# Optimization experiments

Hardware: AMD Instinct MI355X
Metric: run time of the kernel (lower is better)

## Reference

```python
import jax, jax.numpy as jnp
import numpy as np

BEAM_WIDTH = 5  # degenerate: all beams share the same per-step topk, so best beam == greedy argmax path
BLANK = 0


def setup_inputs() -> dict:
    key = jax.random.key(0)
    N, C, T = 128, 128, 2048
    logits = jax.random.normal(key, (N, C, T), dtype=jnp.float32)
    return {"logits": logits}


def reference(logits) -> jnp.ndarray:
    # (N, C, T) -> (N, T, C), log-softmax over classes (matches F.log_softmax(dim=2))
    log_probs = jax.nn.log_softmax(jnp.transpose(logits, (0, 2, 1)), axis=2)
    N, T, C = log_probs.shape
    # Beam search in the source is degenerate: every beam expands with the identical
    # per-timestep top-k, so the highest-scoring beam is exactly the per-step argmax.
    tokens = jnp.argmax(log_probs, axis=2).astype(jnp.int32)  # (N, T)
    # CTC-style collapse (decode()): drop blanks and repeated tokens.
    prev = jnp.concatenate([jnp.full((N, 1), -1, dtype=jnp.int32), tokens[:, :-1]], axis=1)
    keep = (tokens != BLANK) & (tokens != prev)  # (N, T) bool
    # Left-compact kept tokens into a blank-padded (N, T) output.
    pos = jnp.cumsum(keep, axis=1) - 1            # target position if kept
    pos = jnp.where(keep, pos, T)                 # dropped tokens -> dump slot T
    out = jnp.full((N, T + 1), BLANK, dtype=jnp.int32)
    out = out.at[jnp.arange(N)[:, None], pos].set(tokens)
    return out[:, :T]
```

## Files before the change

kernel.cpp:

```cpp
#include <hip/hip_runtime.h>


constexpr int N = 128;
constexpr int C = 128;
constexpr int T = 2048;

__global__ __launch_bounds__(256) void argmax_kernel(const float* __restrict__ logits,
                                                     int* __restrict__ tokens) {
    __shared__ float sb[3][4][64];
    __shared__ int   si[3][4][64];

    const int tid = threadIdx.x;
    const int tq  = tid & 63;
    const int grp = tid >> 6;
    const int b   = blockIdx.x;
    const int n   = b >> 3;
    const int t4  = (b & 7) * 256 + tq * 4;

    const float* base = logits + (size_t)n * C * T + (size_t)(grp * 32) * T + t4;

    float4 best = make_float4(-__builtin_inff(), -__builtin_inff(),
                              -__builtin_inff(), -__builtin_inff());
    int4 bidx = make_int4(0, 0, 0, 0);

    #pragma unroll
    for (int cc = 0; cc < 32; cc += 8) {
        float4 v[8];
        #pragma unroll
        for (int j = 0; j < 8; ++j)
            v[j] = *(const float4*)(base + (size_t)(cc + j) * T);
        #pragma unroll
        for (int j = 0; j < 8; ++j) {
            const int c = cc + j;
            if (v[j].x > best.x) { best.x = v[j].x; bidx.x = c; }
            if (v[j].y > best.y) { best.y = v[j].y; bidx.y = c; }
            if (v[j].z > best.z) { best.z = v[j].z; bidx.z = c; }
            if (v[j].w > best.w) { best.w = v[j].w; bidx.w = c; }
        }
    }

    if (grp > 0) {
        sb[grp - 1][0][tq] = best.x; si[grp - 1][0][tq] = bidx.x + grp * 32;
        sb[grp - 1][1][tq] = best.y; si[grp - 1][1][tq] = bidx.y + grp * 32;
        sb[grp - 1][2][tq] = best.z; si[grp - 1][2][tq] = bidx.z + grp * 32;
        sb[grp - 1][3][tq] = best.w; si[grp - 1][3][tq] = bidx.w + grp * 32;
    }
    __syncthreads();
    if (grp == 0) {
        #pragma unroll
        for (int g = 0; g < 3; ++g) {
            float f;
            f = sb[g][0][tq]; if (f > best.x) { best.x = f; bidx.x = si[g][0][tq]; }
            f = sb[g][1][tq]; if (f > best.y) { best.y = f; bidx.y = si[g][1][tq]; }
            f = sb[g][2][tq]; if (f > best.z) { best.z = f; bidx.z = si[g][2][tq]; }
            f = sb[g][3][tq]; if (f > best.w) { best.w = f; bidx.w = si[g][3][tq]; }
        }
        *(int4*)(tokens + (size_t)n * T + t4) = bidx;
    }
}

__global__ __launch_bounds__(256) void collapse_kernel(const int* __restrict__ tokens,
                                                       int* __restrict__ out) {
    const int n = blockIdx.x;
    const int* trow = tokens + (size_t)n * T;
    int* orow = out + (size_t)n * T;
    const int tid = threadIdx.x;
    constexpr int PER = T / 256;
    const int t0 = tid * PER;

    int tok[PER];
    *(int4*)&tok[0] = *(const int4*)(trow + t0);
    *(int4*)&tok[4] = *(const int4*)(trow + t0 + 4);
    int prev = (t0 == 0) ? -1 : trow[t0 - 1];

    int kpos[PER];
    int cnt = 0;
    #pragma unroll
    for (int i = 0; i < PER; ++i) {
        const bool k = (tok[i] != 0) && (tok[i] != prev);
        kpos[i] = k ? cnt : -1;
        cnt += k ? 1 : 0;
        prev = tok[i];
    }

    const int lane = tid & 63;
    const int wid  = tid >> 6;
    int incl = cnt;
    #pragma unroll
    for (int d = 1; d < 64; d <<= 1) {
        int v = __shfl_up(incl, d, 64);
        if (lane >= d) incl += v;
    }

    __shared__ int wsum[4];
    if (lane == 63) wsum[wid] = incl;

    const int4 z = make_int4(0, 0, 0, 0);
    *(int4*)(orow + t0)     = z;
    *(int4*)(orow + t0 + 4) = z;

    __syncthreads();

    int wbase = 0;
    #pragma unroll
    for (int w = 0; w < 4; ++w)
        if (w < wid) wbase += wsum[w];
    const int base2 = wbase + (incl - cnt);

    #pragma unroll
    for (int i = 0; i < PER; ++i) {
        if (kpos[i] >= 0) orow[base2 + kpos[i]] = tok[i];
    }
}

extern "C" void kernel_launch(void* const* d_in, const int* in_sizes, int n_in,
                              void* d_out, int out_size, void* d_ws, size_t ws_size,
                              hipStream_t stream) {
    const float* logits = (const float*)d_in[0];
    int* out = (int*)d_out;
    int* tokens = (int*)d_ws;

    argmax_kernel<<<N * 8, 256, 0, stream>>>(logits, tokens);
    collapse_kernel<<<N, 256, 0, stream>>>(tokens, out);
}
```

Baseline: 27.76 us.

## Fuse argmax and collapse via last-block-done atomic counter per row

Merges the argmax and CTC-collapse kernels into one launch. Each block bumps a per-row atomic counter after writing its tokens, and the last of the eight blocks for a row runs the collapse scan. This removes the second kernel launch and its dependency gap. In exchange it adds a memset of the counters, thread fences, and a serialized collapse tail on whichever block finishes last.

```diff
diff --git a/kernel.cpp b/kernel.cpp
--- a/kernel.cpp
+++ b/kernel.cpp
@@ -4,11 +4,15 @@
 constexpr int N = 128;
 constexpr int C = 128;
 constexpr int T = 2048;
+constexpr int BPR = 8;
 
-__global__ __launch_bounds__(256) void argmax_kernel(const float* __restrict__ logits,
-                                                     int* __restrict__ tokens) {
+__global__ __launch_bounds__(256) void fused_kernel(const float* __restrict__ logits,
+                                                    int* __restrict__ tokens,
+                                                    int* __restrict__ cnt,
+                                                    int* __restrict__ out) {
     __shared__ float sb[3][4][64];
     __shared__ int   si[3][4][64];
+    __shared__ int   sdone;
 
     const int tid = threadIdx.x;
     const int tq  = tid & 63;
@@ -57,14 +61,19 @@
         }
         *(int4*)(tokens + (size_t)n * T + t4) = bidx;
     }
-}
 
-__global__ __launch_bounds__(256) void collapse_kernel(const int* __restrict__ tokens,
-                                                       int* __restrict__ out) {
-    const int n = blockIdx.x;
+    __syncthreads();
+    if (tid == 0) {
+        __threadfence();
+        const int old = atomicAdd(&cnt[n], 1);
+        sdone = (old == BPR - 1);
+    }
+    __syncthreads();
+    if (!sdone) return;
+    __threadfence();
+
     const int* trow = tokens + (size_t)n * T;
     int* orow = out + (size_t)n * T;
-    const int tid = threadIdx.x;
     constexpr int PER = T / 256;
     const int t0 = tid * PER;
 
@@ -74,18 +83,18 @@
     int prev = (t0 == 0) ? -1 : trow[t0 - 1];
 
     int kpos[PER];
-    int cnt = 0;
+    int cntk = 0;
     #pragma unroll
     for (int i = 0; i < PER; ++i) {
         const bool k = (tok[i] != 0) && (tok[i] != prev);
-        kpos[i] = k ? cnt : -1;
-        cnt += k ? 1 : 0;
+        kpos[i] = k ? cntk : -1;
+        cntk += k ? 1 : 0;
         prev = tok[i];
     }
 
     const int lane = tid & 63;
     const int wid  = tid >> 6;
-    int incl = cnt;
+    int incl = cntk;
     #pragma unroll
     for (int d = 1; d < 64; d <<= 1) {
         int v = __shfl_up(incl, d, 64);
@@ -105,7 +114,7 @@
     #pragma unroll
     for (int w = 0; w < 4; ++w)
         if (w < wid) wbase += wsum[w];
-    const int base2 = wbase + (incl - cnt);
+    const int base2 = wbase + (incl - cntk);
 
     #pragma unroll
     for (int i = 0; i < PER; ++i) {
@@ -119,7 +128,8 @@
     const float* logits = (const float*)d_in[0];
     int* out = (int*)d_out;
     int* tokens = (int*)d_ws;
+    int* cnt = (int*)((char*)d_ws + (size_t)N * T * sizeof(int));
 
-    argmax_kernel<<<N * 8, 256, 0, stream>>>(logits, tokens);
-    collapse_kernel<<<N, 256, 0, stream>>>(tokens, out);
+    hipMemsetAsync(cnt, 0, N * sizeof(int), stream);
+    fused_kernel<<<N * BPR, 256, 0, stream>>>(logits, tokens, cnt, out);
 }
```

After: 99.71 us. 3.59x slower.
